# Performance work log

Hardware: AMD Instinct MI355X
Metric: run time of the kernel (lower is better)

## Reference

```python
import jax, jax.numpy as jnp
import numpy as np

N_NODES = 100000
D = 256
HIDDEN = 256
E = 262144


def setup_inputs() -> dict:
    key = jax.random.key(0)
    ks = jax.random.split(key, 8)
    x_src = jax.random.normal(ks[0], (N_NODES, D), dtype=jnp.float32)
    x_dst = jax.random.normal(ks[1], (N_NODES, D), dtype=jnp.float32)
    # MLP params: Linear(in_src+in_dst -> hidden), ReLU, Linear(hidden -> 1)
    W1 = jax.random.normal(ks[2], (2 * D, HIDDEN), dtype=jnp.float32) * (1.0 / np.sqrt(2 * D))
    b1 = jnp.zeros((HIDDEN,), dtype=jnp.float32)
    W2 = jax.random.normal(ks[3], (HIDDEN, 1), dtype=jnp.float32) * (1.0 / np.sqrt(HIDDEN))
    b2 = jnp.zeros((1,), dtype=jnp.float32)
    edge_index = jax.random.randint(ks[4], (2, E), 0, N_NODES, dtype=jnp.int64)
    neg_edge_index = jax.random.randint(ks[5], (2, E), 0, N_NODES, dtype=jnp.int64)
    return {"x_src": x_src, "x_dst": x_dst, "W1": W1, "b1": b1, "W2": W2,
            "b2": b2, "edge_index": edge_index, "neg_edge_index": neg_edge_index}


def _score(xs, xd, W1, b1, W2, b2):
    # MLP scorer: cat -> Linear -> ReLU -> Linear -> squeeze
    h = jnp.concatenate([xs, xd], axis=-1) @ W1 + b1   # [E, HIDDEN]
    h = jax.nn.relu(h)
    return (h @ W2 + b2).squeeze(-1)                   # [E]


def reference(x_src, x_dst, W1, b1, W2, b2, edge_index, neg_edge_index):
    src, dst = edge_index[0], edge_index[1]
    nsrc, ndst = neg_edge_index[0], neg_edge_index[1]
    pos = _score(x_src[src], x_dst[dst], W1, b1, W2, b2)
    neg = _score(x_src[nsrc], x_dst[ndst], W1, b1, W2, b2)
    return pos, neg
```

## Files before the change

### kernel.cpp

```cpp
#include <hip/hip_runtime.h>

#define D_IN   256
#define HID    256
#define NNODES 100000
#define NEDGE  262144

typedef short short8            __attribute__((ext_vector_type(8)));
typedef float float4v           __attribute__((ext_vector_type(4)));
typedef unsigned short ushort8  __attribute__((ext_vector_type(8)));

__device__ __forceinline__ unsigned short f32_to_bf16_rne(float f) {
    unsigned int u = __float_as_uint(f);
    unsigned int r = u + 0x7FFFu + ((u >> 16) & 1u);
    return (unsigned short)(r >> 16);
}
__device__ __forceinline__ float bf16_to_f32(unsigned short h) {
    return __uint_as_float(((unsigned int)h) << 16);
}

__global__ __launch_bounds__(256) void convert_w(
    const float* __restrict__ W1, unsigned short* __restrict__ Wt)
{
    __shared__ float tile[64][65];
    const int z = blockIdx.z, kb = blockIdx.x * 64, nb = blockIdx.y * 64;
    const int t = threadIdx.x;
    const int g = t >> 6, c = t & 63;
#pragma unroll
    for (int r = 0; r < 16; r++) {
        int kl = g * 16 + r;
        tile[kl][c] = W1[((size_t)(z * 256 + kb + kl)) * 256 + nb + c];
    }
    __syncthreads();
#pragma unroll
    for (int r = 0; r < 16; r++) {
        int nl = g * 16 + r;
        Wt[((size_t)(z * 256 + nb + nl)) * 256 + kb + c] = f32_to_bf16_rne(tile[c][nl]);
    }
}

#define SA 72

__global__ __launch_bounds__(512) void gemm_xw_mfma(
    const float* __restrict__ Xsrc, const float* __restrict__ Xdst,
    const unsigned short* __restrict__ Wt, const float* __restrict__ b1,
    unsigned short* __restrict__ U, unsigned short* __restrict__ V)
{
    const int zz = blockIdx.z;
    const float* X = zz ? Xdst : Xsrc;
    const unsigned short* Wz = Wt + (size_t)zz * 256 * 256;
    unsigned short* C = zz ? V : U;

    const int m0 = blockIdx.x * 128;

    __shared__ __align__(16) unsigned short smem[27648];
    unsigned short* As = smem;
    unsigned short* Bs = smem + 9216;

    const int t = threadIdx.x;
    const int w = t >> 6, lane = t & 63;
    const int wm = w >> 2, wn = w & 3;
    const int quad = lane >> 4, l16 = lane & 15;

    float4v acc[4][4];
#pragma unroll
    for (int mi = 0; mi < 4; mi++)
#pragma unroll
        for (int ni = 0; ni < 4; ni++) acc[mi][ni] = (float4v){0.f, 0.f, 0.f, 0.f};

    for (int ks = 0; ks < D_IN; ks += 64) {
#pragma unroll
        for (int i = 0; i < 4; i++) {
            int s = t + i * 512;
            int row = s >> 4, c4 = (s & 15) << 2;
            int gr = m0 + row; if (gr >= NNODES) gr = NNODES - 1;
            float4 a = *(const float4*)(X + (size_t)gr * D_IN + ks + c4);
            ushort4 p;
            p.x = f32_to_bf16_rne(a.x); p.y = f32_to_bf16_rne(a.y);
            p.z = f32_to_bf16_rne(a.z); p.w = f32_to_bf16_rne(a.w);
            *(ushort4*)(As + row * SA + c4) = p;
        }
#pragma unroll
        for (int i = 0; i < 4; i++) {
            int s = t + i * 512;
            int n = s >> 3, seg = s & 7;
            *(int4*)(Bs + n * SA + seg * 8) =
                *(const int4*)(Wz + (size_t)n * 256 + ks + seg * 8);
        }
        __syncthreads();
#pragma unroll
        for (int kk = 0; kk < 64; kk += 32) {
            short8 af[4], bf[4];
#pragma unroll
            for (int mi = 0; mi < 4; mi++)
                af[mi] = *(const short8*)(As + (wm * 64 + mi * 16 + l16) * SA + kk + quad * 8);
#pragma unroll
            for (int ni = 0; ni < 4; ni++)
                bf[ni] = *(const short8*)(Bs + (wn * 64 + ni * 16 + l16) * SA + kk + quad * 8);
#pragma unroll
            for (int mi = 0; mi < 4; mi++)
#pragma unroll
                for (int ni = 0; ni < 4; ni++)
                    acc[mi][ni] = __builtin_amdgcn_mfma_f32_16x16x32_bf16(
                        af[mi], bf[ni], acc[mi][ni], 0, 0, 0);
        }
        __syncthreads();
    }

    float bias[4];
#pragma unroll
    for (int ni = 0; ni < 4; ni++)
        bias[ni] = (zz == 0) ? b1[wn * 64 + ni * 16 + l16] : 0.f;

    unsigned short* Cs = smem;
#pragma unroll
    for (int h = 0; h < 2; h++) {
        if ((wn >> 1) == h) {
#pragma unroll
            for (int mi = 0; mi < 4; mi++)
#pragma unroll
                for (int ni = 0; ni < 4; ni++) {
                    int cl = (wn & 1) * 64 + ni * 16 + l16;
#pragma unroll
                    for (int r = 0; r < 4; r++) {
                        int row = wm * 64 + mi * 16 + quad * 4 + r;
                        Cs[row * 136 + cl] = f32_to_bf16_rne(acc[mi][ni][r] + bias[ni]);
                    }
                }
        }
        __syncthreads();
#pragma unroll
        for (int i = 0; i < 4; i++) {
            int s = t + i * 512;
            int row = s >> 4, seg = s & 15;
            int gr = m0 + row;
            if (gr < NNODES)
                *(int4*)(C + (size_t)gr * HID + h * 128 + seg * 8) =
                    *(const int4*)(Cs + row * 136 + seg * 8);
        }
        __syncthreads();
    }
}

__global__ __launch_bounds__(256) void edge_score_bf16(
    const unsigned short* __restrict__ U, const unsigned short* __restrict__ V,
    const float* __restrict__ W2, const float* __restrict__ b2,
    const int* __restrict__ epos, const int* __restrict__ eneg,
    float* __restrict__ out)
{
    const int w = threadIdx.x >> 6, lane = threadIdx.x & 63;
    const int half = lane >> 5, hl = lane & 31;
    const int ebase = blockIdx.x * 64 + w * 16;

    const int* ei = (ebase < NEDGE) ? epos : eneg;
    const int eb2 = (ebase < NEDGE) ? ebase : ebase - NEDGE;

    int sidx[8], didx[8];
#pragma unroll
    for (int p = 0; p < 8; p++) {
        int e = eb2 + 2 * p + half;
        sidx[p] = ei[e];
        didx[p] = ei[NEDGE + e];
    }
    ushort8 uu[8], vv[8];
#pragma unroll
    for (int p = 0; p < 8; p++)
        uu[p] = *(const ushort8*)(U + (size_t)sidx[p] * HID + hl * 8);
#pragma unroll
    for (int p = 0; p < 8; p++)
        vv[p] = *(const ushort8*)(V + (size_t)didx[p] * HID + hl * 8);

    float w2r[8];
    *(float4*)&w2r[0] = *(const float4*)(W2 + hl * 8);
    *(float4*)&w2r[4] = *(const float4*)(W2 + hl * 8 + 4);
    const float bb2 = b2[0];

#pragma unroll
    for (int p = 0; p < 8; p++) {
        float s = 0.f;
#pragma unroll
        for (int q = 0; q < 8; q++)
            s += fmaxf(bf16_to_f32(uu[p][q]) + bf16_to_f32(vv[p][q]), 0.f) * w2r[q];
#pragma unroll
        for (int off = 16; off; off >>= 1)
            s += __shfl_xor(s, off, 64);
        if (hl == 0) out[ebase + 2 * p + half] = s + bb2;
    }
}

__global__ __launch_bounds__(256) void edge_score_direct(
    const float* __restrict__ xs_, const float* __restrict__ xd_,
    const float* __restrict__ W1, const float* __restrict__ b1,
    const float* __restrict__ W2, const float* __restrict__ b2,
    const int* __restrict__ epos, const int* __restrict__ eneg,
    float* __restrict__ out)
{
    __shared__ float xrow[2 * D_IN];
    __shared__ float red[256];
    const int e = blockIdx.x;
    const int* ei = (e < NEDGE) ? epos : eneg;
    const int e2  = (e < NEDGE) ? e : e - NEDGE;
    const int s = ei[e2];
    const int d = ei[NEDGE + e2];
    const int t = threadIdx.x;

    xrow[t]        = xs_[(size_t)s * D_IN + t];
    xrow[D_IN + t] = xd_[(size_t)d * D_IN + t];
    __syncthreads();

    float acc = b1[t];
    for (int k = 0; k < 2 * D_IN; k++)
        acc += xrow[k] * W1[(size_t)k * HID + t];
    acc = fmaxf(acc, 0.f);
    red[t] = acc * W2[t];
    __syncthreads();
    for (int st = 128; st; st >>= 1) {
        if (t < st) red[t] += red[t + st];
        __syncthreads();
    }
    if (t == 0) out[e] = red[0] + b2[0];
}

extern "C" void kernel_launch(void* const* d_in, const int* in_sizes, int n_in,
                              void* d_out, int out_size, void* d_ws, size_t ws_size,
                              hipStream_t stream) {
    const float* x_src = (const float*)d_in[0];
    const float* x_dst = (const float*)d_in[1];
    const float* W1    = (const float*)d_in[2];
    const float* b1    = (const float*)d_in[3];
    const float* W2    = (const float*)d_in[4];
    const float* b2    = (const float*)d_in[5];
    const int*   epos  = (const int*)d_in[6];
    const int*   eneg  = (const int*)d_in[7];
    float* out = (float*)d_out;

    const size_t uv   = (size_t)NNODES * HID;
    const size_t need = (2 * uv + 2 * 256 * 256) * sizeof(unsigned short);
    if (ws_size >= need) {
        unsigned short* U  = (unsigned short*)d_ws;
        unsigned short* V  = U + uv;
        unsigned short* Wt = V + uv;
        convert_w<<<dim3(4, 4, 2), 256, 0, stream>>>(W1, Wt);
        dim3 g1((NNODES + 127) / 128, 1, 2);
        gemm_xw_mfma<<<g1, 512, 0, stream>>>(x_src, x_dst, Wt, b1, U, V);
        edge_score_bf16<<<(2 * NEDGE) / 64, 256, 0, stream>>>(U, V, W2, b2, epos, eneg, out);
    } else {
        edge_score_direct<<<2 * NEDGE, 256, 0, stream>>>(x_src, x_dst, W1, b1, W2, b2, epos, eneg, out);
    }
}
```

Measured before the change: 334.9 us.

## Load full W tile into LDS once and stream A fragments directly from global

The GEMM kernel now loads the entire 256x256 bf16 weight slice into shared memory once per block. Each wave reads its A fragments straight from global fp32 into registers, converting to bf16 with a cheaper round-half-up, instead of staging A through LDS. This removes the per-k-step A staging and its barriers, and adds a min-2-blocks occupancy hint. In exchange the block uses about 132KB of LDS, so fewer blocks fit per CU. Each lane's global A loads are also less coalesced, and every wave column re-reads the same A rows, adding redundant global traffic.

Result: slower. 412.9 us (+23.3%).

```diff
diff --git a/kernel.cpp b/kernel.cpp
--- a/kernel.cpp
+++ b/kernel.cpp
@@ -14,6 +14,9 @@
     unsigned int r = u + 0x7FFFu + ((u >> 16) & 1u);
     return (unsigned short)(r >> 16);
 }
+__device__ __forceinline__ unsigned short f32_to_bf16_rnu(float f) {
+    return (unsigned short)((__float_as_uint(f) + 0x8000u) >> 16);
+}
 __device__ __forceinline__ float bf16_to_f32(unsigned short h) {
     return __uint_as_float(((unsigned int)h) << 16);
 }
@@ -38,9 +41,9 @@
     }
 }
 
-#define SA 72
-
-__global__ __launch_bounds__(512) void gemm_xw_mfma(
+#define BSTR 264
+
+__global__ __launch_bounds__(512, 2) void gemm_xw_mfma(
     const float* __restrict__ Xsrc, const float* __restrict__ Xdst,
     const unsigned short* __restrict__ Wt, const float* __restrict__ b1,
     unsigned short* __restrict__ U, unsigned short* __restrict__ V)
@@ -52,58 +55,60 @@
 
     const int m0 = blockIdx.x * 128;
 
-    __shared__ __align__(16) unsigned short smem[27648];
-    unsigned short* As = smem;
-    unsigned short* Bs = smem + 9216;
+    __shared__ __align__(16) unsigned short smem[256 * BSTR];
+    unsigned short* Bs = smem;
 
     const int t = threadIdx.x;
     const int w = t >> 6, lane = t & 63;
     const int wm = w >> 2, wn = w & 3;
     const int quad = lane >> 4, l16 = lane & 15;
 
+#pragma unroll
+    for (int i = 0; i < 16; i++) {
+        int c = t + i * 512;
+        int n = c >> 5, s = (c & 31) << 3;
+        *(int4*)(Bs + n * BSTR + s) = *(const int4*)(Wz + (size_t)n * 256 + s);
+    }
+
+    const float* arow[4];
+#pragma unroll
+    for (int mi = 0; mi < 4; mi++) {
+        int gr = m0 + wm * 64 + mi * 16 + l16;
+        if (gr >= NNODES) gr = NNODES - 1;
+        arow[mi] = X + (size_t)gr * D_IN + quad * 8;
+    }
+
     float4v acc[4][4];
 #pragma unroll
     for (int mi = 0; mi < 4; mi++)
 #pragma unroll
         for (int ni = 0; ni < 4; ni++) acc[mi][ni] = (float4v){0.f, 0.f, 0.f, 0.f};
 
-    for (int ks = 0; ks < D_IN; ks += 64) {
-#pragma unroll
-        for (int i = 0; i < 4; i++) {
-            int s = t + i * 512;
-            int row = s >> 4, c4 = (s & 15) << 2;
-            int gr = m0 + row; if (gr >= NNODES) gr = NNODES - 1;
-            float4 a = *(const float4*)(X + (size_t)gr * D_IN + ks + c4);
-            ushort4 p;
-            p.x = f32_to_bf16_rne(a.x); p.y = f32_to_bf16_rne(a.y);
-            p.z = f32_to_bf16_rne(a.z); p.w = f32_to_bf16_rne(a.w);
-            *(ushort4*)(As + row * SA + c4) = p;
+    __syncthreads();
+
+#pragma unroll
+    for (int ks = 0; ks < D_IN; ks += 32) {
+        short8 af[4], bf[4];
+#pragma unroll
+        for (int mi = 0; mi < 4; mi++) {
+            float4 a0 = *(const float4*)(arow[mi] + ks);
+            float4 a1 = *(const float4*)(arow[mi] + ks + 4);
+            short8 v;
+            v[0] = (short)f32_to_bf16_rnu(a0.x); v[1] = (short)f32_to_bf16_rnu(a0.y);
+            v[2] = (short)f32_to_bf16_rnu(a0.z); v[3] = (short)f32_to_bf16_rnu(a0.w);
+            v[4] = (short)f32_to_bf16_rnu(a1.x); v[5] = (short)f32_to_bf16_rnu(a1.y);
+            v[6] = (short)f32_to_bf16_rnu(a1.z); v[7] = (short)f32_to_bf16_rnu(a1.w);
+            af[mi] = v;
         }
 #pragma unroll
-        for (int i = 0; i < 4; i++) {
-            int s = t + i * 512;
-            int n = s >> 3, seg = s & 7;
-            *(int4*)(Bs + n * SA + seg * 8) =
-                *(const int4*)(Wz + (size_t)n * 256 + ks + seg * 8);
-        }
-        __syncthreads();
-#pragma unroll
-        for (int kk = 0; kk < 64; kk += 32) {
-            short8 af[4], bf[4];
-#pragma unroll
-            for (int mi = 0; mi < 4; mi++)
-                af[mi] = *(const short8*)(As + (wm * 64 + mi * 16 + l16) * SA + kk + quad * 8);
+        for (int ni = 0; ni < 4; ni++)
+            bf[ni] = *(const short8*)(Bs + (wn * 64 + ni * 16 + l16) * BSTR + ks + quad * 8);
+#pragma unroll
+        for (int mi = 0; mi < 4; mi++)
 #pragma unroll
             for (int ni = 0; ni < 4; ni++)
-                bf[ni] = *(const short8*)(Bs + (wn * 64 + ni * 16 + l16) * SA + kk + quad * 8);
-#pragma unroll
-            for (int mi = 0; mi < 4; mi++)
-#pragma unroll
-                for (int ni = 0; ni < 4; ni++)
-                    acc[mi][ni] = __builtin_amdgcn_mfma_f32_16x16x32_bf16(
-                        af[mi], bf[ni], acc[mi][ni], 0, 0, 0);
-        }
-        __syncthreads();
+                acc[mi][ni] = __builtin_amdgcn_mfma_f32_16x16x32_bf16(
+                    af[mi], bf[ni], acc[mi][ni], 0, 0, 0);
     }
 
     float bias[4];
@@ -111,6 +116,7 @@
     for (int ni = 0; ni < 4; ni++)
         bias[ni] = (zz == 0) ? b1[wn * 64 + ni * 16 + l16] : 0.f;
 
+    __syncthreads();
     unsigned short* Cs = smem;
 #pragma unroll
     for (int h = 0; h < 2; h++) {
```
